# Kernel optimization log

Hardware: AMD Instinct MI355X
Metric: run time of the kernel (lower is better)

The kernel has to match this reference:

```python
import jax, jax.numpy as jnp
import numpy as np

N, D, V, T = 1024, 64, 32000, 2048
U_DECAY = 0.97
LN_EPS = 1e-6


def _layernorm_row(z):
    # matches torch: (z - mean) / (std_unbiased + eps), std uses ddof=1
    m = z.mean(axis=-1, keepdims=True)
    s = jnp.std(z, axis=-1, ddof=1, keepdims=True)
    return (z - m) / (s + LN_EPS)


def setup_inputs() -> dict:
    key = jax.random.key(0)
    k1, k2, k3, k4, k5 = jax.random.split(key, 5)
    E = jax.random.normal(k1, (D, N), dtype=jnp.float32) / np.float32(np.sqrt(N))
    Dx = jax.random.normal(k2, (N, D), dtype=jnp.float32) / np.float32(np.sqrt(D))
    Dy = jax.random.normal(k3, (N, D), dtype=jnp.float32) / np.float32(np.sqrt(D))
    token_emb = jax.random.normal(k4, (V, D), dtype=jnp.float32) / np.float32(np.sqrt(D))
    tokens = jax.random.randint(k5, (T,), 0, V, dtype=jnp.int32)
    x0 = jnp.zeros((N,), dtype=jnp.float32)
    rho0 = jnp.zeros((D, N), dtype=jnp.float32)
    return {"E": E, "Dx": Dx, "Dy": Dy, "token_emb": token_emb,
            "x0": x0, "rho0": rho0, "tokens": tokens}


def reference(E, Dx, Dy, token_emb, x0, rho0, tokens):
    def step(carry, tok):
        x, rho = carry                        # x: [N], rho: [D, N]
        v_prev = token_emb[tok]               # [D]
        x_t = x + jax.nn.relu(Dx @ v_prev)    # [N], use_relu_lowrank=True
        a_star = rho @ x_t                    # [D]
        y_core = Dy @ _layernorm_row(a_star)  # ln_before_Dy=True -> [N]
        y_t = jax.nn.relu(y_core) * jax.nn.relu(x_t)  # [N]
        v_star = _layernorm_row(E @ y_t)      # [D]
        rho_new = U_DECAY * (rho + jnp.outer(v_prev, x_t))  # [D, N]
        return (x_t, rho_new), (y_t, v_star)

    (_, _), (ys, vs) = jax.lax.scan(step, (x0, rho0), tokens)
    return ys, vs  # [T, N], [T, D]
```

## Files before the change

### kernel.cpp

```cpp
#include <hip/hip_runtime.h>
#include <math.h>

#define NN 1024
#define DD 64
#define TT 2048
#define UDEC 0.97f
#define EPS 1e-6f

#define CC 64
#define NCH 32
#define NSL 16
#define SLW 64
#define C2 8
#define NC2 256

#define NTHR 256

__device__ __forceinline__ int swz4(int r, int c4) { return r * 16 + (c4 ^ (r & 15)); }

#define DOT4(p, q2) ((p).x*(q2).x + (p).y*(q2).y + (p).z*(q2).z + (p).w*(q2).w)
#define F4ADD(a, b) make_float4((a).x+(b).x, (a).y+(b).y, (a).z+(b).z, (a).w+(b).w)

__global__ __launch_bounds__(NTHR) void k_prep(
    const float* __restrict__ E, float* __restrict__ Et4,
    const float* __restrict__ Dx, float* __restrict__ Dxq,
    const float* __restrict__ Dy, float* __restrict__ Dyq)
{
    const int b = blockIdx.x, tid = threadIdx.x;
    if (b < 64) {
        const int fi = b * NTHR + tid;
        const int n4 = fi >> 6, d = fi & 63;
        reinterpret_cast<float4*>(Et4)[fi] =
            reinterpret_cast<const float4*>(E)[d * (NN / 4) + n4];
    } else if (b < 128) {
        const int fi = (b - 64) * NTHR + tid;
        const int d4 = fi >> 10, n = fi & 1023;
        reinterpret_cast<float4*>(Dxq)[fi] =
            reinterpret_cast<const float4*>(Dx)[n * (DD / 4) + d4];
    } else {
        const int fi = (b - 128) * NTHR + tid;
        const int d4 = fi >> 10, n = fi & 1023;
        reinterpret_cast<float4*>(Dyq)[fi] =
            reinterpret_cast<const float4*>(Dy)[n * (DD / 4) + d4];
    }
}

__global__ __launch_bounds__(NTHR) void k_xscan(
    const float* __restrict__ Dxq, const float* __restrict__ temb,
    const int* __restrict__ toks, float* __restrict__ Xp, float* __restrict__ S)
{
    __shared__ float Vs[C2][DD];
    const int b = blockIdx.x, tid = threadIdx.x;
    const int cs = b >> 2, qx = b & 3;
    const int n = qx * 256 + tid;
    for (int i = tid; i < C2 * DD / 4; i += NTHR) {
        int s = i >> 4, d4 = i & 15;
        reinterpret_cast<float4*>(&Vs[s][0])[d4] =
            reinterpret_cast<const float4*>(temb + toks[cs * C2 + s] * DD)[d4];
    }
    __syncthreads();
    float dxr[DD];
    const float4* dxq4 = reinterpret_cast<const float4*>(Dxq);
#pragma unroll
    for (int j = 0; j < 16; ++j) {
        float4 v = dxq4[j * NN + n];
        dxr[4*j] = v.x; dxr[4*j+1] = v.y; dxr[4*j+2] = v.z; dxr[4*j+3] = v.w;
    }
    float run = 0.f;
    for (int s = 0; s < C2; ++s) {
        const float4* vr = reinterpret_cast<const float4*>(&Vs[s][0]);
        float a0 = 0.f, a1 = 0.f, a2 = 0.f, a3 = 0.f;
#pragma unroll
        for (int j = 0; j < 16; ++j) {
            float4 v = vr[j];
            a0 += v.x * dxr[4*j];     a1 += v.y * dxr[4*j+1];
            a2 += v.z * dxr[4*j+2];   a3 += v.w * dxr[4*j+3];
        }
        run += fmaxf((a0 + a1) + (a2 + a3), 0.f);
        Xp[(cs * C2 + s) * NN + n] = run;
    }
    S[cs * NN + n] = run;
}

__global__ __launch_bounds__(NTHR) void k_base(
    const float* __restrict__ S, const float* __restrict__ x0, float* __restrict__ Bb)
{
    __shared__ float ssl[8][33];
    const int b = blockIdx.x, tid = threadIdx.x;
    const int n_l = tid & 31, seg = tid >> 5;
    const int n = b * 32 + n_l;
    float m[32];
#pragma unroll
    for (int j = 0; j < 32; ++j) m[j] = S[(seg * 32 + j) * NN + n];
    float tot = 0.f;
#pragma unroll
    for (int j = 0; j < 32; ++j) tot += m[j];
    ssl[seg][n_l] = tot;
    __syncthreads();
    float acc = x0[n];
    for (int r = 0; r < seg; ++r) acc += ssl[r][n_l];
#pragma unroll
    for (int j = 0; j < 32; ++j) {
        Bb[(seg * 32 + j) * NN + n] = acc;
        acc += m[j];
    }
}

__global__ __launch_bounds__(NTHR) void k_mgram(
    const float* __restrict__ Xp, const float* __restrict__ Bb,
    const float* __restrict__ temb, const int* __restrict__ toks,
    float* __restrict__ M, float* __restrict__ Gp)
{
    __shared__ float Xs[CC * DD];
    __shared__ float Vw[CC * DD];
    __shared__ float pw[CC + 1];
    const int b = blockIdx.x, tid = threadIdx.x;
    const int c = b >> 5, q = (b >> 1) & 15, role = b & 1;
    if (role == 0 && tid <= CC) pw[tid] = powf(UDEC, (float)tid);
    for (int i = tid; i < CC * SLW / 4; i += NTHR) {
        int s = i >> 4, n4 = i & 15;
        int t = c * CC + s;
        float4 xv = *reinterpret_cast<const float4*>(&Xp[t * NN + q * SLW + n4 * 4]);
        float4 bv = *reinterpret_cast<const float4*>(&Bb[(t >> 3) * NN + q * SLW + n4 * 4]);
        reinterpret_cast<float4*>(Xs)[swz4(s, n4)] = F4ADD(xv, bv);
    }
    __syncthreads();
    if (role == 0) {
        for (int i = tid; i < CC * DD / 4; i += NTHR) {
            int s = i >> 4, d4 = i & 15;
            float4 v = reinterpret_cast<const float4*>(temb + toks[c * CC + s] * DD)[d4];
            float wv = pw[CC - s];
            reinterpret_cast<float4*>(Vw)[swz4(s, d4)] =
                make_float4(v.x * wv, v.y * wv, v.z * wv, v.w * wv);
        }
    }
    __syncthreads();
    const float4* Xs4 = reinterpret_cast<const float4*>(Xs);
    if (role == 0) {
        const int dg = tid >> 4, ng = tid & 15;
        float acc[16];
#pragma unroll
        for (int k = 0; k < 16; ++k) acc[k] = 0.f;
        const float4* Vw4 = reinterpret_cast<const float4*>(Vw);
        for (int s = 0; s < CC; ++s) {
            float4 vw = Vw4[swz4(s, dg)];
            float4 xs = Xs4[swz4(s, ng)];
            acc[0]  += vw.x*xs.x; acc[1]  += vw.x*xs.y; acc[2]  += vw.x*xs.z; acc[3]  += vw.x*xs.w;
            acc[4]  += vw.y*xs.x; acc[5]  += vw.y*xs.y; acc[6]  += vw.y*xs.z; acc[7]  += vw.y*xs.w;
            acc[8]  += vw.z*xs.x; acc[9]  += vw.z*xs.y; acc[10] += vw.z*xs.z; acc[11] += vw.z*xs.w;
            acc[12] += vw.w*xs.x; acc[13] += vw.w*xs.y; acc[14] += vw.w*xs.z; acc[15] += vw.w*xs.w;
        }
#pragma unroll
        for (int a = 0; a < 4; ++a)
            *reinterpret_cast<float4*>(&M[(c * DD + dg * 4 + a) * NN + q * SLW + ng * 4]) =
                make_float4(acc[a*4], acc[a*4+1], acc[a*4+2], acc[a*4+3]);
    } else {
        const int tg = tid >> 4, sg = tid & 15;
        float acc[16];
#pragma unroll
        for (int k = 0; k < 16; ++k) acc[k] = 0.f;
        for (int n4 = 0; n4 < 16; ++n4) {
            float4 xa[4], xb[4];
#pragma unroll
            for (int a = 0; a < 4; ++a) xa[a] = Xs4[swz4(tg * 4 + a, n4)];
#pragma unroll
            for (int e = 0; e < 4; ++e) xb[e] = Xs4[swz4(sg * 4 + e, n4)];
#pragma unroll
            for (int a = 0; a < 4; ++a)
#pragma unroll
                for (int e = 0; e < 4; ++e) acc[a*4+e] += DOT4(xa[a], xb[e]);
        }
        float* base = Gp + ((size_t)(c * NSL + q) * CC) * CC;
#pragma unroll
        for (int a = 0; a < 4; ++a)
            *reinterpret_cast<float4*>(base + (tg * 4 + a) * CC + sg * 4) =
                make_float4(acc[a*4], acc[a*4+1], acc[a*4+2], acc[a*4+3]);
    }
}

__global__ __launch_bounds__(NTHR) void k_rho(
    const float* __restrict__ M, const float* __restrict__ rho0, float* __restrict__ Rho)
{
    __shared__ float4 ssl[8][32];
    const int b = blockIdx.x, tid = threadIdx.x;
    const int l = tid & 31, seg = tid >> 5;
    const int f = b * 32 + l;
    const float uc  = powf(UDEC, (float)CC);
    const float uc4 = uc * uc * uc * uc;
    const float4* M4 = reinterpret_cast<const float4*>(M);
    float4 mreg[4];
#pragma unroll
    for (int j = 0; j < 4; ++j) mreg[j] = M4[(size_t)(seg * 4 + j) * (DD * NN / 4) + f];
    float4 ss = mreg[0];
#pragma unroll
    for (int j = 1; j < 4; ++j) {
        ss.x = fmaf(ss.x, uc, mreg[j].x); ss.y = fmaf(ss.y, uc, mreg[j].y);
        ss.z = fmaf(ss.z, uc, mreg[j].z); ss.w = fmaf(ss.w, uc, mreg[j].w);
    }
    ssl[seg][l] = ss;
    __syncthreads();
    float4 acc = reinterpret_cast<const float4*>(rho0)[f];
    for (int r = 0; r < seg; ++r) {
        float4 sv = ssl[r][l];
        acc.x = fmaf(acc.x, uc4, sv.x); acc.y = fmaf(acc.y, uc4, sv.y);
        acc.z = fmaf(acc.z, uc4, sv.z); acc.w = fmaf(acc.w, uc4, sv.w);
    }
    float4* R4 = reinterpret_cast<float4*>(Rho);
#pragma unroll
    for (int j = 0; j < 4; ++j) {
        R4[(size_t)(seg * 4 + j) * (DD * NN / 4) + f] = acc;
        acc.x = fmaf(acc.x, uc, mreg[j].x); acc.y = fmaf(acc.y, uc, mreg[j].y);
        acc.z = fmaf(acc.z, uc, mreg[j].z); acc.w = fmaf(acc.w, uc, mreg[j].w);
    }
}

__global__ __launch_bounds__(NTHR) void k_inter(
    const float* __restrict__ Xp, const float* __restrict__ Bb,
    const float* __restrict__ Rho, float* __restrict__ Pp)
{
    __shared__ float Xs[32 * DD];
    __shared__ float Rs[DD * DD];
    const int b = blockIdx.x, tid = threadIdx.x;
    const int c = b >> 5, q = (b >> 1) & 15, h = b & 1;
    for (int i = tid; i < 32 * SLW / 4; i += NTHR) {
        int s = i >> 4, n4 = i & 15;
        int t = c * CC + h * 32 + s;
        float4 xv = *reinterpret_cast<const float4*>(&Xp[t * NN + q * SLW + n4 * 4]);
        float4 bv = *reinterpret_cast<const float4*>(&Bb[(t >> 3) * NN + q * SLW + n4 * 4]);
        reinterpret_cast<float4*>(Xs)[swz4(s, n4)] = F4ADD(xv, bv);
    }
    for (int i = tid; i < DD * SLW / 4; i += NTHR) {
        int s = i >> 4, n4 = i & 15;
        reinterpret_cast<float4*>(Rs)[swz4(s, n4)] =
            *reinterpret_cast<const float4*>(&Rho[(size_t)(c * DD + s) * NN + q * SLW + n4 * 4]);
    }
    __syncthreads();
    const float4* Xs4 = reinterpret_cast<const float4*>(Xs);
    const float4* Rs4 = reinterpret_cast<const float4*>(Rs);
    const int ti = tid >> 4, dg = tid & 15;
    float acc[8];
#pragma unroll
    for (int k = 0; k < 8; ++k) acc[k] = 0.f;
    for (int n4 = 0; n4 < 16; ++n4) {
        float4 xa[2], rv[4];
#pragma unroll
        for (int a = 0; a < 2; ++a) xa[a] = Xs4[swz4(ti * 2 + a, n4)];
#pragma unroll
        for (int e = 0; e < 4; ++e) rv[e] = Rs4[swz4(dg * 4 + e, n4)];
#pragma unroll
        for (int a = 0; a < 2; ++a)
#pragma unroll
            for (int e = 0; e < 4; ++e) acc[a*4+e] += DOT4(xa[a], rv[e]);
    }
#pragma unroll
    for (int a = 0; a < 2; ++a) {
        int trow = h * 32 + ti * 2 + a;
        *reinterpret_cast<float4*>(
            Pp + (((size_t)(c * NSL + q) * CC) + trow) * DD + dg * 4) =
            make_float4(acc[a*4], acc[a*4+1], acc[a*4+2], acc[a*4+3]);
    }
}

__global__ __launch_bounds__(NTHR) void k_astar(
    const float* __restrict__ Gp, const float* __restrict__ Pp,
    const float* __restrict__ temb, const int* __restrict__ toks,
    float* __restrict__ LNA)
{
    __shared__ float Ve[CC * DD];
    __shared__ float Gt[4][CC];
    __shared__ float Pt[4][DD];
    __shared__ float pw[CC + 1];
    const int b = blockIdx.x, tid = threadIdx.x;
    const int c = b >> 4, sub = b & 15;
    if (tid <= CC) pw[tid] = powf(UDEC, (float)tid);
    for (int i = tid; i < CC * DD / 4; i += NTHR) {
        int s = i >> 4, d4 = i & 15;
        reinterpret_cast<float4*>(Ve)[s * 16 + d4] =
            reinterpret_cast<const float4*>(temb + toks[c * CC + s] * DD)[d4];
    }
    {
        int k = tid >> 6, s = tid & 63;
        int t = sub + 16 * k;
        float ag = 0.f, ap = 0.f;
#pragma unroll
        for (int q = 0; q < NSL; ++q) {
            ag += Gp[((size_t)(c * NSL + q) * CC + t) * CC + s];
            ap += Pp[((size_t)(c * NSL + q) * CC + t) * DD + s];
        }
        Gt[k][s] = ag; Pt[k][s] = ap;
    }
    __syncthreads();
    {
        const int tk = tid >> 6, d0 = tid & 63;
        const int t = sub + 16 * tk;
        float a = pw[t] * Pt[tk][d0];
        for (int s = 0; s < t; ++s)
            a = fmaf(pw[t - s] * Gt[tk][s], Ve[s * 64 + d0], a);
        float sum = a;
#pragma unroll
        for (int mm = 1; mm < 64; mm <<= 1) sum += __shfl_xor(sum, mm, 64);
        float mean = sum * (1.f / DD);
        float z = a - mean;
        float vv = z * z;
#pragma unroll
        for (int mm = 1; mm < 64; mm <<= 1) vv += __shfl_xor(vv, mm, 64);
        float inv = 1.f / (sqrtf(vv * (1.f / (DD - 1))) + EPS);
        LNA[(c * CC + t) * DD + d0] = z * inv;
    }
}

__global__ __launch_bounds__(NTHR) void k_yv(
    const float* __restrict__ LNA, const float* __restrict__ Dyq,
    const float* __restrict__ Xp, const float* __restrict__ Bb,
    const float* __restrict__ Et4, float* __restrict__ ys, float* __restrict__ vs)
{
    __shared__ float L[4][DD];
    __shared__ float Ys[4][NN];
    __shared__ float pre4[4][4][DD];
    __shared__ float pre[4][DD + 1];
    __shared__ float mrow[4], srow[4];
    const int tt = blockIdx.x, tid = threadIdx.x;
    if (tid < 64) {
        reinterpret_cast<float4*>(&L[0][0])[tid] =
            reinterpret_cast<const float4*>(LNA + tt * 4 * DD)[tid];
    }
    __syncthreads();
    const float4* dyq4 = reinterpret_cast<const float4*>(Dyq);
    for (int nq = 0; nq < 4; ++nq) {
        const int n = nq * 256 + tid;
        float dyr[DD];
#pragma unroll
        for (int j = 0; j < 16; ++j) {
            float4 v = dyq4[j * NN + n];
            dyr[4*j] = v.x; dyr[4*j+1] = v.y; dyr[4*j+2] = v.z; dyr[4*j+3] = v.w;
        }
#pragma unroll
        for (int k = 0; k < 4; ++k) {
            const float4* lr = reinterpret_cast<const float4*>(&L[k][0]);
            float a0 = 0.f, a1 = 0.f, a2 = 0.f, a3 = 0.f;
#pragma unroll
            for (int j = 0; j < 16; ++j) {
                float4 v = lr[j];
                a0 += v.x * dyr[4*j];   a1 += v.y * dyr[4*j+1];
                a2 += v.z * dyr[4*j+2]; a3 += v.w * dyr[4*j+3];
            }
            float yc = (a0 + a1) + (a2 + a3);
            int tg = tt * 4 + k;
            float xv = Xp[tg * NN + n] + Bb[(tg >> 3) * NN + n];
            float yv = fmaxf(yc, 0.f) * fmaxf(xv, 0.f);
            ys[tg * NN + n] = yv;
            Ys[k][n] = yv;
        }
    }
    __syncthreads();
    const int w = tid >> 6, d = tid & 63;
    float a0 = 0.f, a1 = 0.f, a2 = 0.f, a3 = 0.f;
    const float4* et = reinterpret_cast<const float4*>(Et4) + (size_t)w * 64 * DD + d;
#pragma unroll 4
    for (int i = 0; i < 64; ++i) {
        float4 ev = et[(size_t)i * DD];
        const int n4g = (w * 64 + i) * 4;
        float4 y0 = *reinterpret_cast<const float4*>(&Ys[0][n4g]);
        float4 y1 = *reinterpret_cast<const float4*>(&Ys[1][n4g]);
        float4 y2 = *reinterpret_cast<const float4*>(&Ys[2][n4g]);
        float4 y3 = *reinterpret_cast<const float4*>(&Ys[3][n4g]);
        a0 += DOT4(ev, y0); a1 += DOT4(ev, y1);
        a2 += DOT4(ev, y2); a3 += DOT4(ev, y3);
    }
    pre4[w][0][d] = a0; pre4[w][1][d] = a1;
    pre4[w][2][d] = a2; pre4[w][3][d] = a3;
    __syncthreads();
    {
        const int k = tid >> 6, dd = tid & 63;
        pre[k][dd] = pre4[0][k][dd] + pre4[1][k][dd] + pre4[2][k][dd] + pre4[3][k][dd];
    }
    __syncthreads();
    if (tid < 4) {
        float m = 0.f;
#pragma unroll
        for (int dd2 = 0; dd2 < DD; ++dd2) m += pre[tid][dd2];
        m *= (1.f / DD);
        float v = 0.f;
#pragma unroll
        for (int dd2 = 0; dd2 < DD; ++dd2) { float z = pre[tid][dd2] - m; v += z * z; }
        mrow[tid] = m;
        srow[tid] = 1.f / (sqrtf(v * (1.f / (DD - 1))) + EPS);
    }
    __syncthreads();
    {
        int k = tid >> 6, dd = tid & 63;
        vs[(tt * 4 + k) * DD + dd] = (pre[k][dd] - mrow[k]) * srow[k];
    }
}

extern "C" void kernel_launch(void* const* d_in, const int* in_sizes, int n_in,
                              void* d_out, int out_size, void* d_ws, size_t ws_size,
                              hipStream_t stream) {
    (void)in_sizes; (void)n_in; (void)out_size; (void)ws_size;
    const float* E    = (const float*)d_in[0];
    const float* Dx   = (const float*)d_in[1];
    const float* Dy   = (const float*)d_in[2];
    const float* temb = (const float*)d_in[3];
    const float* x0   = (const float*)d_in[4];
    const float* rho0 = (const float*)d_in[5];
    const int*   toks = (const int*)d_in[6];

    float* ys = (float*)d_out;
    float* vs = ys + (size_t)TT * NN;

    float* w   = (float*)d_ws;
    float* Xp  = w;
    float* S   = Xp  + (size_t)TT * NN;
    float* Bb  = S   + (size_t)NC2 * NN;
    float* M   = Bb  + (size_t)NC2 * NN;
    float* Rho = M   + (size_t)NCH * DD * NN;
    float* Gp  = Rho + (size_t)NCH * DD * NN;
    float* LNA = Gp  + (size_t)NCH * NSL * CC * CC;
    float* Et4 = LNA + (size_t)TT * DD;
    float* Dxq = Et4 + (size_t)NN * DD;
    float* Dyq = Dxq + (size_t)NN * DD;
    float* Pp  = M;

    k_prep <<<dim3(192),       NTHR, 0, stream>>>(E, Et4, Dx, Dxq, Dy, Dyq);
    k_xscan<<<dim3(4 * NC2),   NTHR, 0, stream>>>(Dxq, temb, toks, Xp, S);
    k_base <<<dim3(32),        NTHR, 0, stream>>>(S, x0, Bb);
    k_mgram<<<dim3(NCH*NSL*2), NTHR, 0, stream>>>(Xp, Bb, temb, toks, M, Gp);
    k_rho  <<<dim3(512),       NTHR, 0, stream>>>(M, rho0, Rho);
    k_inter<<<dim3(NCH*NSL*2), NTHR, 0, stream>>>(Xp, Bb, Rho, Pp);
    k_astar<<<dim3(NCH*16),    NTHR, 0, stream>>>(Gp, Pp, temb, toks, LNA);
    k_yv   <<<dim3(TT/4),      NTHR, 0, stream>>>(LNA, Dyq, Xp, Bb, Et4, ys, vs);
}
```

Measured before the change: 180.9 us.

## Split fused y/v kernel into separate y and v kernels with wider grid

```diff
diff --git a/kernel.cpp b/kernel.cpp
--- a/kernel.cpp
+++ b/kernel.cpp
@@ -309,49 +309,53 @@
     }
 }
 
-__global__ __launch_bounds__(NTHR) void k_yv(
+__global__ __launch_bounds__(NTHR) void k_y(
     const float* __restrict__ LNA, const float* __restrict__ Dyq,
     const float* __restrict__ Xp, const float* __restrict__ Bb,
-    const float* __restrict__ Et4, float* __restrict__ ys, float* __restrict__ vs)
-{
-    __shared__ float L[4][DD];
+    float* __restrict__ ys)
+{
+    __shared__ float L[8][DD];
+    const int tt = blockIdx.y;
+    const int n  = blockIdx.x * 256 + threadIdx.x;
+    for (int i = threadIdx.x; i < 8 * DD / 4; i += NTHR)
+        reinterpret_cast<float4*>(&L[0][0])[i] =
+            reinterpret_cast<const float4*>(LNA + tt * 8 * DD)[i];
+    __syncthreads();
+    float dyr[DD];
+    const float4* dyq4 = reinterpret_cast<const float4*>(Dyq);
+#pragma unroll
+    for (int j = 0; j < 16; ++j) {
+        float4 v = dyq4[j * NN + n];
+        dyr[4*j] = v.x; dyr[4*j+1] = v.y; dyr[4*j+2] = v.z; dyr[4*j+3] = v.w;
+    }
+#pragma unroll
+    for (int t = 0; t < 8; ++t) {
+        const float4* lr = reinterpret_cast<const float4*>(&L[t][0]);
+        float a0 = 0.f, a1 = 0.f, a2 = 0.f, a3 = 0.f;
+#pragma unroll
+        for (int j = 0; j < 16; ++j) {
+            float4 v = lr[j];
+            a0 += v.x * dyr[4*j];   a1 += v.y * dyr[4*j+1];
+            a2 += v.z * dyr[4*j+2]; a3 += v.w * dyr[4*j+3];
+        }
+        float yc = (a0 + a1) + (a2 + a3);
+        int tg = tt * 8 + t;
+        float xv = Xp[tg * NN + n] + Bb[(tg >> 3) * NN + n];
+        ys[tg * NN + n] = fmaxf(yc, 0.f) * fmaxf(xv, 0.f);
+    }
+}
+
+__global__ __launch_bounds__(NTHR) void k_v(
+    const float* __restrict__ ys, const float* __restrict__ Et4, float* __restrict__ vs)
+{
     __shared__ float Ys[4][NN];
     __shared__ float pre4[4][4][DD];
     __shared__ float pre[4][DD + 1];
     __shared__ float mrow[4], srow[4];
     const int tt = blockIdx.x, tid = threadIdx.x;
-    if (tid < 64) {
-        reinterpret_cast<float4*>(&L[0][0])[tid] =
-            reinterpret_cast<const float4*>(LNA + tt * 4 * DD)[tid];
-    }
-    __syncthreads();
-    const float4* dyq4 = reinterpret_cast<const float4*>(Dyq);
-    for (int nq = 0; nq < 4; ++nq) {
-        const int n = nq * 256 + tid;
-        float dyr[DD];
-#pragma unroll
-        for (int j = 0; j < 16; ++j) {
-            float4 v = dyq4[j * NN + n];
-            dyr[4*j] = v.x; dyr[4*j+1] = v.y; dyr[4*j+2] = v.z; dyr[4*j+3] = v.w;
-        }
-#pragma unroll
-        for (int k = 0; k < 4; ++k) {
-            const float4* lr = reinterpret_cast<const float4*>(&L[k][0]);
-            float a0 = 0.f, a1 = 0.f, a2 = 0.f, a3 = 0.f;
-#pragma unroll
-            for (int j = 0; j < 16; ++j) {
-                float4 v = lr[j];
-                a0 += v.x * dyr[4*j];   a1 += v.y * dyr[4*j+1];
-                a2 += v.z * dyr[4*j+2]; a3 += v.w * dyr[4*j+3];
-            }
-            float yc = (a0 + a1) + (a2 + a3);
-            int tg = tt * 4 + k;
-            float xv = Xp[tg * NN + n] + Bb[(tg >> 3) * NN + n];
-            float yv = fmaxf(yc, 0.f) * fmaxf(xv, 0.f);
-            ys[tg * NN + n] = yv;
-            Ys[k][n] = yv;
-        }
-    }
+    for (int i = tid; i < NN; i += NTHR)
+        reinterpret_cast<float4*>(&Ys[0][0])[i] =
+            reinterpret_cast<const float4*>(ys + (size_t)tt * 4 * NN)[i];
     __syncthreads();
     const int w = tid >> 6, d = tid & 63;
     float a0 = 0.f, a1 = 0.f, a2 = 0.f, a3 = 0.f;
@@ -428,5 +432,6 @@
     k_rho  <<<dim3(512),       NTHR, 0, stream>>>(M, rho0, Rho);
     k_inter<<<dim3(NCH*NSL*2), NTHR, 0, stream>>>(Xp, Bb, Rho, Pp);
     k_astar<<<dim3(NCH*16),    NTHR, 0, stream>>>(Gp, Pp, temb, toks, LNA);
-    k_yv   <<<dim3(TT/4),      NTHR, 0, stream>>>(LNA, Dyq, Xp, Bb, Et4, ys, vs);
-}
+    k_y    <<<dim3(4, TT/8),   NTHR, 0, stream>>>(LNA, Dyq, Xp, Bb, ys);
+    k_v    <<<dim3(TT/4),      NTHR, 0, stream>>>(ys, Et4, vs);
+}
```

Result: faster. 157.4 us (-13.0%).
